# Kernel tuning notes

Measured on AMD Instinct MI355X. Metric: run time of the kernel, lower is better.

## Reference

```python
import jax, jax.numpy as jnp
import numpy as np

NUM_HEADS = 8
DIM_HEAD = 64
SCALE = DIM_HEAD * NUM_HEADS  # q *= dim_head * num_heads, as in the source


def setup_inputs() -> dict:
    key = jax.random.key(0)
    k1, k2, k3, k4 = jax.random.split(key, 4)
    B, C, H, W = 8, 64, 32, 32
    x = jax.random.normal(k1, (B, C, H, W), dtype=jnp.float32)
    # 1x1 conv == matmul over channels; small init keeps post-scale logits sane
    w_qkv = jax.random.normal(k2, (3 * NUM_HEADS * DIM_HEAD, C), dtype=jnp.float32) * 0.02
    rel_h = jax.random.normal(k3, (2 * H - 1, DIM_HEAD), dtype=jnp.float32) * 0.02
    rel_w = jax.random.normal(k4, (2 * W - 1, DIM_HEAD), dtype=jnp.float32) * 0.02
    return {"x": x, "w_qkv": w_qkv, "rel_h": rel_h, "rel_w": rel_w}


def _rel_indices(H, W):
    # flattened 2D grid positions
    pos_y = np.repeat(np.arange(H), W)  # [HW]
    pos_x = np.tile(np.arange(W), H)    # [HW]
    rel_y = pos_y[None, :] - pos_y[:, None] + (H - 1)  # [HW, HW] in [0, 2H-2]
    rel_x = pos_x[None, :] - pos_x[:, None] + (W - 1)  # [HW, HW] in [0, 2W-2]
    return jnp.asarray(rel_y), jnp.asarray(rel_x)


def reference(x, w_qkv, rel_h, rel_w):
    B, C, H, W = x.shape
    n = H * W
    # 1x1 conv (bias=False) -> per-pixel matmul
    xf = x.reshape(B, C, n)                              # b c n
    qkv = jnp.einsum('oc,bcn->bon', w_qkv, xf)           # b (3 h d) n
    q, k, v = jnp.split(qkv, 3, axis=1)
    def to_heads(t):  # b (h d) n -> b h n d
        return t.reshape(B, NUM_HEADS, DIM_HEAD, n).transpose(0, 1, 3, 2)
    q, k, v = to_heads(q), to_heads(k), to_heads(v)
    q = q * SCALE  # scale applied before QK^T AND before pos bias (in-place in torch)

    sim = jnp.einsum('bhid,bhjd->bhij', q, k)            # [B, h, n, n]

    # relative position bias: q_i . rel_h[dy] + q_i . rel_w[dx]
    logits_h = jnp.einsum('bhid,rd->bhir', q, rel_h)     # [B, h, n, 2H-1]
    logits_w = jnp.einsum('bhid,rd->bhir', q, rel_w)     # [B, h, n, 2W-1]
    rel_y, rel_x = _rel_indices(H, W)                    # [n, n] each
    i_idx = jnp.arange(n)[:, None]                       # [n, 1]
    bias = logits_h[:, :, i_idx, rel_y] + logits_w[:, :, i_idx, rel_x]  # [B,h,n,n]

    attn = jax.nn.softmax(sim + bias, axis=-1)
    out = jnp.einsum('bhij,bhjd->bhid', attn, v)         # [B, h, n, d]
    out = out.transpose(0, 1, 3, 2).reshape(B, NUM_HEADS * DIM_HEAD, H, W)
    return out
```

## Files before the change

kernel.cpp:

```cpp
#include <hip/hip_runtime.h>
#include <hip/hip_bf16.h>
#include <hip/hip_fp16.h>

typedef _Float16 h8 __attribute__((ext_vector_type(8)));
typedef _Float16 h2 __attribute__((ext_vector_type(2)));
typedef unsigned short us8 __attribute__((ext_vector_type(8)));
typedef float f4 __attribute__((ext_vector_type(4)));
typedef float f16v __attribute__((ext_vector_type(16)));

#define NH 8
#define DH 64
#define NPIX 1024
#define CIN 64
#define NBH 64
#define QSCALE (512.0f * 1.44269504f)
#define LOSCALE 2048.0f
#define INV_LOSCALE (1.0f / 2048.0f)
#define DTHR 12.0f

__device__ __forceinline__ void gload_lds16(const void* g, void* lds) {
  __builtin_amdgcn_global_load_lds(
      (const __attribute__((address_space(1))) void*)g,
      (__attribute__((address_space(3))) void*)lds, 16, 0, 0);
}

__device__ __forceinline__ float fexp2(float x) {
#if __has_builtin(__builtin_amdgcn_exp2f)
  return __builtin_amdgcn_exp2f(x);
#else
  return exp2f(x);
#endif
}

__device__ __forceinline__ unsigned pk16(float a, float b) {
  auto r = __builtin_amdgcn_cvt_pkrtz(a, b);
  union { decltype(r) h; unsigned u; } x;
  x.h = r;
  return x.u;
}

__global__ __launch_bounds__(256) void qkv_mfma(
    const float* __restrict__ x, const float* __restrict__ wqkv,
    _Float16* __restrict__ Qh, _Float16* __restrict__ Ql,
    _Float16* __restrict__ Kh, _Float16* __restrict__ Kl,
    _Float16* __restrict__ Vv) {
  __shared__ __align__(16) char QS[49152];
  char* Wh = QS;
  char* Wl = QS + 16384;
  char* Xh = QS + 32768;
  char* Xl = QS + 40960;

  const int tid = threadIdx.x;
  const int lane = tid & 63;
  const int w = tid >> 6;
  const int c = lane & 15;
  const int g = lane >> 4;
  const int o0 = blockIdx.x * 128;
  const int p0 = blockIdx.y * 64;
  const int b = blockIdx.z;

  #pragma unroll
  for (int it = 0; it < 4; ++it) {
    int task = tid + it * 256;
    int oct = task & 7, o = task >> 3;
    const f4* wr = (const f4*)(wqkv + (size_t)(o0 + o) * CIN + oct * 8);
    f4 wa = wr[0], wb = wr[1];
    h8 hi, lo;
    #pragma unroll
    for (int e = 0; e < 8; ++e) {
      float v = e < 4 ? wa[e] : wb[e - 4];
      _Float16 h = (_Float16)v;
      hi[e] = h;
      lo[e] = (_Float16)((v - (float)h) * LOSCALE);
    }
    int byo = o * 128 + ((oct ^ (o & 7)) << 4);
    *(h8*)(Wh + byo) = hi;
    *(h8*)(Wl + byo) = lo;
  }
  {
    int kp = tid & 31;
    int pgrp = tid >> 5;
    const float* xr0 = x + ((size_t)b * CIN + 2 * kp) * NPIX + p0 + pgrp * 8;
    const float* xr1 = xr0 + NPIX;
    f4 a0 = *(const f4*)xr0, a1 = *(const f4*)(xr0 + 4);
    f4 b0 = *(const f4*)xr1, b1 = *(const f4*)(xr1 + 4);
    int oct = kp >> 2;
    int slot4 = (kp & 3) * 4;
    #pragma unroll
    for (int e = 0; e < 8; ++e) {
      float v0 = e < 4 ? a0[e] : a1[e - 4];
      float v1 = e < 4 ? b0[e] : b1[e - 4];
      _Float16 h0 = (_Float16)v0, h1 = (_Float16)v1;
      float l0f = (v0 - (float)h0) * LOSCALE;
      float l1f = (v1 - (float)h1) * LOSCALE;
      int p = pgrp * 8 + e;
      int byo = p * 128 + ((oct ^ (p & 7)) << 4) + slot4;
      union { h2 h; unsigned u; } uh, ul;
      uh.h[0] = h0; uh.h[1] = h1;
      ul.h[0] = (_Float16)l0f; ul.h[1] = (_Float16)l1f;
      *(unsigned*)(Xh + byo) = uh.u;
      *(unsigned*)(Xl + byo) = ul.u;
    }
  }
  __syncthreads();

  f4 zf = {0.f, 0.f, 0.f, 0.f};
  f4 acc[2][4], cor[2][4];
  #pragma unroll
  for (int oi = 0; oi < 2; ++oi)
    #pragma unroll
    for (int pi = 0; pi < 4; ++pi) { acc[oi][pi] = zf; cor[oi][pi] = zf; }

  const int ob = w * 32;
  #pragma unroll
  for (int kh = 0; kh < 2; ++kh) {
    h8 ah[2], al[2], bh[4], bl[4];
    #pragma unroll
    for (int oi = 0; oi < 2; ++oi) {
      int orow = ob + ((c >> 2) << 3) + (c & 3) + oi * 4;
      int ch = (((kh * 4 + g) ^ (orow & 7)) << 4);
      ah[oi] = *(const h8*)(Wh + orow * 128 + ch);
      al[oi] = *(const h8*)(Wl + orow * 128 + ch);
    }
    #pragma unroll
    for (int pi = 0; pi < 4; ++pi) {
      int prow = pi * 16 + c;
      int ch = (((kh * 4 + g) ^ (prow & 7)) << 4);
      bh[pi] = *(const h8*)(Xh + prow * 128 + ch);
      bl[pi] = *(const h8*)(Xl + prow * 128 + ch);
    }
    __builtin_amdgcn_s_setprio(1);
    #pragma unroll
    for (int oi = 0; oi < 2; ++oi)
      #pragma unroll
      for (int pi = 0; pi < 4; ++pi) {
        acc[oi][pi] = __builtin_amdgcn_mfma_f32_16x16x32_f16(ah[oi], bh[pi], acc[oi][pi], 0, 0, 0);
        cor[oi][pi] = __builtin_amdgcn_mfma_f32_16x16x32_f16(ah[oi], bl[pi], cor[oi][pi], 0, 0, 0);
        cor[oi][pi] = __builtin_amdgcn_mfma_f32_16x16x32_f16(al[oi], bh[pi], cor[oi][pi], 0, 0, 0);
      }
    __builtin_amdgcn_s_setprio(0);
  }

  const int part = o0 >> 9;
  const float scl = part == 0 ? QSCALE : 1.0f;
  _Float16* dsth = part == 0 ? Qh : (part == 1 ? Kh : Vv);
  _Float16* dstl = part == 0 ? Ql : (part == 1 ? Kl : nullptr);
  #pragma unroll
  for (int pi = 0; pi < 4; ++pi) {
    int obase = o0 + ob + 8 * g;
    int h = (obase >> 6) & 7;
    int d = obase & 63;
    int p_abs = p0 + pi * 16 + c;
    size_t off = (((size_t)(b * NH + h)) * NPIX + p_abs) * DH + d;
    h8 hv, lv;
    #pragma unroll
    for (int oi = 0; oi < 2; ++oi)
      #pragma unroll
      for (int reg = 0; reg < 4; ++reg) {
        float v = (acc[oi][pi][reg] + cor[oi][pi][reg] * INV_LOSCALE) * scl;
        _Float16 hh = (_Float16)v;
        hv[oi * 4 + reg] = hh;
        lv[oi * 4 + reg] = (_Float16)(v - (float)hh);
      }
    *(h8*)(dsth + off) = hv;
    if (dstl) *(h8*)(dstl + off) = lv;
  }
}

__global__ __launch_bounds__(256, 2) void attn_mfma(
    const _Float16* __restrict__ Qh, const _Float16* __restrict__ Ql,
    const _Float16* __restrict__ Kh, const _Float16* __restrict__ Kl,
    const _Float16* __restrict__ V,
    const float* __restrict__ rel_h, const float* __restrict__ rel_w,
    float* __restrict__ out) {
  __shared__ __align__(16) char SMem[73728];
  _Float16* LHc = (_Float16*)(SMem + 65536);
  _Float16* LWT = (_Float16*)(SMem + 32768);
  float* OT = (float*)SMem;

  const int tid = threadIdx.x;
  const int lane = tid & 63;
  const int w = tid >> 6;
  const int wu = __builtin_amdgcn_readfirstlane(w);
  const int c = lane & 15;
  const int g = lane >> 4;
  const int il = lane & 31;
  const int hi = lane >> 5;
  const int bx = blockIdx.x;
  const int bh = ((bx & 7) << 3) | ((bx >> 3) & 7);
  const int i0 = (bx >> 6) << 7;
  char* SPw = SMem + 49152 + w * 4096;

  const _Float16* Qhg = Qh + (size_t)bh * NPIX * DH;
  const _Float16* Qlg = Ql + (size_t)bh * NPIX * DH;
  const _Float16* Khg = Kh + (size_t)bh * NPIX * DH;
  const _Float16* Klg = Kl + (size_t)bh * NPIX * DH;
  const _Float16* Vg  = V  + (size_t)bh * NPIX * DH;

  const h8* Qr0h = (const h8*)(Qhg + (size_t)(i0 + w * 32 + c) * DH);
  const h8* Qr0l = (const h8*)(Qlg + (size_t)(i0 + w * 32 + c) * DH);
  const h8* Qr1h = (const h8*)(Qhg + (size_t)(i0 + w * 32 + 16 + c) * DH);
  const h8* Qr1l = (const h8*)(Qlg + (size_t)(i0 + w * 32 + 16 + c) * DH);
  h8 q0h[2] = {Qr0h[g], Qr0h[4 + g]};
  h8 q0l[2] = {Qr0l[g], Qr0l[4 + g]};
  h8 q1h[2] = {Qr1h[g], Qr1h[4 + g]};
  h8 q1l[2] = {Qr1l[g], Qr1l[4 + g]};

  const int s0i = wu * 128 + lane;
  const int s1i = s0i + 64;
  const int ko0 = (s0i >> 3) * 128 + (((s0i & 7) ^ ((s0i >> 3) & 7)) << 4);
  const int ko1 = (s1i >> 3) * 128 + (((s1i & 7) ^ ((s1i >> 3) & 7)) << 4);

  #pragma unroll
  for (int it = 0; it < 2; ++it) {
    int task = tid + it * 256;
    int oct = task & 7, s = task >> 3;
    int ss = s < 63 ? s : 62;
    const float* sh = rel_h + (size_t)ss * DH + oct * 8;
    const float* sw = rel_w + (size_t)ss * DH + oct * 8;
    h8 hh, ww;
    #pragma unroll
    for (int e = 0; e < 8; ++e) {
      hh[e] = (_Float16)sh[e];
      ww[e] = (_Float16)sw[e];
    }
    int byo = s * 128 + ((oct ^ (s & 7)) << 4);
    *(h8*)(SMem + byo) = hh;
    *(h8*)(SMem + 16384 + byo) = ww;
  }
  __syncthreads();

  const int yi = (i0 + w * 32) >> 5;
  f4 zf = {0.f, 0.f, 0.f, 0.f};
  #pragma unroll
  for (int rs = 0; rs < 2; ++rs) {
    f4 lhD[4], lwD[4];
    #pragma unroll
    for (int st = 0; st < 4; ++st) { lhD[st] = zf; lwD[st] = zf; }
    #pragma unroll
    for (int kh = 0; kh < 2; ++kh) {
      h8 bq = rs ? q1h[kh] : q0h[kh];
      h8 bl = rs ? q1l[kh] : q0l[kh];
      #pragma unroll
      for (int st = 0; st < 4; ++st) {
        int srow = st * 16 + c;
        int chb = srow * 128 + (((kh * 4 + g) ^ (srow & 7)) << 4);
        h8 ra = *(const h8*)(SMem + chb);
        h8 wa = *(const h8*)(SMem + 16384 + chb);
        lhD[st] = __builtin_amdgcn_mfma_f32_16x16x32_f16(ra, bq, lhD[st], 0, 0, 0);
        lhD[st] = __builtin_amdgcn_mfma_f32_16x16x32_f16(ra, bl, lhD[st], 0, 0, 0);
        lwD[st] = __builtin_amdgcn_mfma_f32_16x16x32_f16(wa, bq, lwD[st], 0, 0, 0);
        lwD[st] = __builtin_amdgcn_mfma_f32_16x16x32_f16(wa, bl, lwD[st], 0, 0, 0);
      }
    }
    int lrow = w * 32 + rs * 16 + c;
    #pragma unroll
    for (int st = 0; st < 4; ++st)
      #pragma unroll
      for (int reg = 0; reg < 4; ++reg) {
        int s = st * 16 + 4 * g + reg;
        int k = s - 31 + yi;
        if (k >= 0 && k < 32)
          LHc[(k >> 1) * 256 + lrow * 2 + (k & 1)] = (_Float16)lhD[st][reg];
        LWT[lrow * 64 + s] = (_Float16)lwD[st][reg];
      }
  }
  __syncthreads();

  float lwp[16];
  {
    int r = w * 32 + il;
    #pragma unroll
    for (int reg = 0; reg < 16; ++reg) {
      int jl = (reg & 3) + 8 * (reg >> 2) + 4 * hi;
      lwp[reg] = (float)LWT[r * 64 + 31 + jl - il];
    }
  }
  const h8* Qmh = (const h8*)(Qhg + (size_t)(i0 + w * 32 + il) * DH);
  const h8* Qml = (const h8*)(Qlg + (size_t)(i0 + w * 32 + il) * DH);
  h8 qmh[4], qml[4];
  #pragma unroll
  for (int kb = 0; kb < 4; ++kb) {
    qmh[kb] = Qmh[2 * kb + hi];
    qml[kb] = Qml[2 * kb + hi];
  }
  __syncthreads();

  {
    gload_lds16((const char*)Khg + ko0, SMem + wu * 2048);
    gload_lds16((const char*)Khg + ko1, SMem + wu * 2048 + 1024);
    gload_lds16((const char*)Klg + ko0, SMem + 16384 + wu * 2048);
    gload_lds16((const char*)Klg + ko1, SMem + 16384 + wu * 2048 + 1024);
    int jp = tid & 31, dd = tid >> 5;
    const h8* vr = (const h8*)(Vg + (size_t)(2 * jp) * DH);
    h8 v0 = vr[dd], v1 = vr[8 + dd];
    us8 u0 = *(const us8*)&v0, u1 = *(const us8*)&v1;
    #pragma unroll
    for (int e = 0; e < 8; ++e) {
      int d = dd * 8 + e;
      unsigned int val = (unsigned int)u0[e] | ((unsigned int)u1[e] << 16);
      *(unsigned int*)(SMem + 32768 + d * 128 + (((jp >> 2) ^ (d & 7)) << 4) + (jp & 3) * 4) = val;
    }
  }
  __syncthreads();

  float m_s = -1e30f, lp = 0.f;
  f16v O0 = {0.f}, O1 = {0.f};
  #pragma unroll
  for (int e = 0; e < 16; ++e) { O0[e] = 0.f; O1[e] = 0.f; }

  const int swl = (il & 7);
  int cur = 0;
  #pragma unroll 1
  for (int t = 0; t < 16; ++t) {
    char* Kc  = SMem + cur * 8192;
    char* KLc = SMem + 16384 + cur * 8192;
    char* Vc  = SMem + 32768 + cur * 8192;
    const int nxt = cur ^ 1;
    const bool pre = t < 15;
    const int jp = tid & 31, dd = tid >> 5;
    h8 v0 = {}, v1 = {};
    if (pre) {
      const char* kg  = (const char*)Khg + (size_t)(t + 1) * 8192;
      const char* klg = (const char*)Klg + (size_t)(t + 1) * 8192;
      gload_lds16(kg + ko0, SMem + nxt * 8192 + wu * 2048);
      gload_lds16(kg + ko1, SMem + nxt * 8192 + wu * 2048 + 1024);
      gload_lds16(klg + ko0, SMem + 16384 + nxt * 8192 + wu * 2048);
      gload_lds16(klg + ko1, SMem + 16384 + nxt * 8192 + wu * 2048 + 1024);
      const h8* vr = (const h8*)(Vg + (size_t)((t + 1) * 64 + 2 * jp) * DH);
      v0 = vr[dd];
      v1 = vr[8 + dd];
    }

    f16v S0 = O0 * 0.f, S1 = O0 * 0.f;
    #pragma unroll
    for (int e = 0; e < 16; ++e) { S0[e] = 0.f; S1[e] = 0.f; }
    #pragma unroll
    for (int kb = 0; kb < 4; ++kb) {
      int chb0 = il * 128 + (((2 * kb + hi) ^ swl) << 4);
      int chb1 = chb0 + 32 * 128;
      h8 a0h = *(const h8*)(Kc + chb0);
      h8 a0l = *(const h8*)(KLc + chb0);
      h8 a1h = *(const h8*)(Kc + chb1);
      h8 a1l = *(const h8*)(KLc + chb1);
      __builtin_amdgcn_s_setprio(1);
      S0 = __builtin_amdgcn_mfma_f32_32x32x16_f16(a0h, qmh[kb], S0, 0, 0, 0);
      S0 = __builtin_amdgcn_mfma_f32_32x32x16_f16(a0l, qmh[kb], S0, 0, 0, 0);
      S0 = __builtin_amdgcn_mfma_f32_32x32x16_f16(a0h, qml[kb], S0, 0, 0, 0);
      S1 = __builtin_amdgcn_mfma_f32_32x32x16_f16(a1h, qmh[kb], S1, 0, 0, 0);
      S1 = __builtin_amdgcn_mfma_f32_32x32x16_f16(a1l, qmh[kb], S1, 0, 0, 0);
      S1 = __builtin_amdgcn_mfma_f32_32x32x16_f16(a1h, qml[kb], S1, 0, 0, 0);
      __builtin_amdgcn_s_setprio(0);
    }

    {
      int r = w * 32 + il;
      h2 lhu = *(const h2*)(LHc + t * 256 + r * 2);
      float lh0 = (float)lhu[0], lh1 = (float)lhu[1];
      #pragma unroll
      for (int reg = 0; reg < 16; ++reg) {
        S0[reg] += lwp[reg] + lh0;
        S1[reg] += lwp[reg] + lh1;
      }
      float v8[8];
      #pragma unroll
      for (int e = 0; e < 8; ++e)
        v8[e] = fmaxf(fmaxf(S0[e], S0[e + 8]), fmaxf(S1[e], S1[e + 8]));
      float w0 = fmaxf(fmaxf(v8[0], v8[1]), fmaxf(v8[2], v8[3]));
      float w1 = fmaxf(fmaxf(v8[4], v8[5]), fmaxf(v8[6], v8[7]));
      float mx = fmaxf(w0, w1);
      mx = fmaxf(mx, __shfl_xor(mx, 32, 64));
      bool sk = mx <= m_s + DTHR;
      if (!__all(sk)) {
        float mn = fmaxf(m_s, mx);
        float corr = fexp2(m_s - mn);
        m_s = mn;
        lp *= corr;
        #pragma unroll
        for (int e = 0; e < 16; ++e) { O0[e] *= corr; O1[e] *= corr; }
      }
      float sum = 0.f;
      char* pbse = SPw + il * 128 + hi * 8;
      #pragma unroll
      for (int a = 0; a < 4; ++a) {
        float p0 = fexp2(S0[4 * a + 0] - m_s);
        float p1 = fexp2(S0[4 * a + 1] - m_s);
        float p2 = fexp2(S0[4 * a + 2] - m_s);
        float p3 = fexp2(S0[4 * a + 3] - m_s);
        sum += (p0 + p1) + (p2 + p3);
        *(unsigned long long*)(pbse + ((a ^ swl) << 4)) =
            (unsigned long long)pk16(p0, p1) | ((unsigned long long)pk16(p2, p3) << 32);
      }
      #pragma unroll
      for (int a = 0; a < 4; ++a) {
        float p0 = fexp2(S1[4 * a + 0] - m_s);
        float p1 = fexp2(S1[4 * a + 1] - m_s);
        float p2 = fexp2(S1[4 * a + 2] - m_s);
        float p3 = fexp2(S1[4 * a + 3] - m_s);
        sum += (p0 + p1) + (p2 + p3);
        *(unsigned long long*)(pbse + (((4 + a) ^ swl) << 4)) =
            (unsigned long long)pk16(p0, p1) | ((unsigned long long)pk16(p2, p3) << 32);
      }
      lp += sum;
    }
    __builtin_amdgcn_wave_barrier();

    #pragma unroll
    for (int jkb = 0; jkb < 4; ++jkb) {
      int ci = 2 * jkb + hi;
      int och = ((ci ^ swl) << 4);
      h8 pb = *(const h8*)(SPw + il * 128 + och);
      __builtin_amdgcn_s_setprio(1);
      h8 av0 = *(const h8*)(Vc + il * 128 + och);
      h8 av1 = *(const h8*)(Vc + (32 + il) * 128 + och);
      O0 = __builtin_amdgcn_mfma_f32_32x32x16_f16(av0, pb, O0, 0, 0, 0);
      O1 = __builtin_amdgcn_mfma_f32_32x32x16_f16(av1, pb, O1, 0, 0, 0);
      __builtin_amdgcn_s_setprio(0);
    }

    if (pre) {
      us8 u0 = *(const us8*)&v0, u1 = *(const us8*)&v1;
      char* Vn = SMem + 32768 + nxt * 8192;
      #pragma unroll
      for (int e = 0; e < 8; ++e) {
        int d = dd * 8 + e;
        unsigned int val = (unsigned int)u0[e] | ((unsigned int)u1[e] << 16);
        *(unsigned int*)(Vn + d * 128 + (((jp >> 2) ^ (d & 7)) << 4) + (jp & 3) * 4) = val;
      }
    }
    __syncthreads();
    cur = nxt;
  }

  float lt = lp + __shfl_xor(lp, 32, 64);
  float rr = __builtin_amdgcn_rcpf(lt);
  {
    int r = w * 32 + il;
    #pragma unroll
    for (int reg = 0; reg < 16; ++reg) {
      int dl = (reg & 3) + 8 * (reg >> 2) + 4 * hi;
      int d0 = dl;
      int d1 = 32 + dl;
      OT[d0 * 128 + (r ^ ((d0 & 7) << 3))] = O0[reg] * rr;
      OT[d1 * 128 + (r ^ ((d1 & 7) << 3))] = O1[reg] * rr;
    }
  }
  __syncthreads();
  #pragma unroll
  for (int it = 0; it < 8; ++it) {
    int task = tid + it * 256;
    int rq = task & 31, d = task >> 5;
    f4 vv = *(const f4*)&OT[d * 128 + ((rq * 4) ^ ((d & 7) << 3))];
    *(f4*)(out + (((size_t)bh * 64 + d) << 10) + i0 + rq * 4) = vv;
  }
}

extern "C" void kernel_launch(void* const* d_in, const int* in_sizes, int n_in,
                              void* d_out, int out_size, void* d_ws, size_t ws_size,
                              hipStream_t stream) {
  const float* x  = (const float*)d_in[0];
  const float* wq = (const float*)d_in[1];
  const float* rh = (const float*)d_in[2];
  const float* rw = (const float*)d_in[3];
  float* out = (float*)d_out;

  const size_t sz = (size_t)NBH * NPIX * DH;
  _Float16* Qh = (_Float16*)d_ws;
  _Float16* Ql = Qh + sz;
  _Float16* Kh = Ql + sz;
  _Float16* Kl = Kh + sz;
  _Float16* V  = Kl + sz;

  qkv_mfma<<<dim3(12, 16, 8), 256, 0, stream>>>(x, wq, Qh, Ql, Kh, Kl, V);
  attn_mfma<<<dim3(512), 256, 0, stream>>>(Qh, Ql, Kh, Kl, V, rh, rw, out);
}
```

Before: 76.01 us.

## Build P operand in registers via permlane32 swap; stage QKV stores through LDS

In the attention kernel, the softmax probabilities are now packed to fp16 and redistributed across lane halves with permlane32_swap to form the MFMA B operand directly. This replaces the per-wave LDS round trip (write P, wave barrier, read back) and shrinks shared memory from 72KB to 56KB, which may allow more resident blocks. In the QKV projection kernel, the output tile is transposed through swizzled LDS so each thread writes contiguous 16-byte chunks along d, aiming for better-coalesced global stores at the cost of two extra block barriers.

```diff
diff --git a/kernel.cpp b/kernel.cpp
--- a/kernel.cpp
+++ b/kernel.cpp
@@ -7,6 +7,7 @@
 typedef unsigned short us8 __attribute__((ext_vector_type(8)));
 typedef float f4 __attribute__((ext_vector_type(4)));
 typedef float f16v __attribute__((ext_vector_type(16)));
+typedef int i2v __attribute__((ext_vector_type(2)));
 
 #define NH 8
 #define DH 64
@@ -49,6 +50,8 @@
   char* Wl = QS + 16384;
   char* Xh = QS + 32768;
   char* Xl = QS + 40960;
+  char* Thi = QS;
+  char* Tlo = QS + 16384;
 
   const int tid = threadIdx.x;
   const int lane = tid & 63;
@@ -145,25 +148,45 @@
   const float scl = part == 0 ? QSCALE : 1.0f;
   _Float16* dsth = part == 0 ? Qh : (part == 1 ? Kh : Vv);
   _Float16* dstl = part == 0 ? Ql : (part == 1 ? Kl : nullptr);
-  #pragma unroll
-  for (int pi = 0; pi < 4; ++pi) {
-    int obase = o0 + ob + 8 * g;
-    int h = (obase >> 6) & 7;
-    int d = obase & 63;
-    int p_abs = p0 + pi * 16 + c;
-    size_t off = (((size_t)(b * NH + h)) * NPIX + p_abs) * DH + d;
-    h8 hv, lv;
-    #pragma unroll
-    for (int oi = 0; oi < 2; ++oi)
-      #pragma unroll
-      for (int reg = 0; reg < 4; ++reg) {
-        float v = (acc[oi][pi][reg] + cor[oi][pi][reg] * INV_LOSCALE) * scl;
-        _Float16 hh = (_Float16)v;
-        hv[oi * 4 + reg] = hh;
-        lv[oi * 4 + reg] = (_Float16)(v - (float)hh);
-      }
-    *(h8*)(dsth + off) = hv;
-    if (dstl) *(h8*)(dstl + off) = lv;
+
+  __syncthreads();
+  {
+    const int chunk = 4 * w + g;
+    #pragma unroll
+    for (int pi = 0; pi < 4; ++pi) {
+      int p = pi * 16 + c;
+      h8 hv, lv;
+      #pragma unroll
+      for (int oi = 0; oi < 2; ++oi)
+        #pragma unroll
+        for (int reg = 0; reg < 4; ++reg) {
+          float v = (acc[oi][pi][reg] + cor[oi][pi][reg] * INV_LOSCALE) * scl;
+          _Float16 hh = (_Float16)v;
+          hv[oi * 4 + reg] = hh;
+          lv[oi * 4 + reg] = (_Float16)(v - (float)hh);
+        }
+      int byo = p * 256 + ((chunk ^ (p & 15)) << 4);
+      *(h8*)(Thi + byo) = hv;
+      if (dstl) *(h8*)(Tlo + byo) = lv;
+    }
+  }
+  __syncthreads();
+  #pragma unroll
+  for (int it = 0; it < 4; ++it) {
+    int task = tid + it * 256;
+    int p = task >> 4;
+    int ck = task & 15;
+    int byo = p * 256 + ((ck ^ (p & 15)) << 4);
+    int o = o0 + ck * 8;
+    int h = (o >> 6) & 7;
+    int d = o & 63;
+    size_t off = (((size_t)(b * NH + h)) * NPIX + p0 + p) * DH + d;
+    h8 v = *(const h8*)(Thi + byo);
+    *(h8*)(dsth + off) = v;
+    if (dstl) {
+      h8 v2 = *(const h8*)(Tlo + byo);
+      *(h8*)(dstl + off) = v2;
+    }
   }
 }
 
@@ -173,8 +196,8 @@
     const _Float16* __restrict__ V,
     const float* __restrict__ rel_h, const float* __restrict__ rel_w,
     float* __restrict__ out) {
-  __shared__ __align__(16) char SMem[73728];
-  _Float16* LHc = (_Float16*)(SMem + 65536);
+  __shared__ __align__(16) char SMem[57344];
+  _Float16* LHc = (_Float16*)(SMem + 49152);
   _Float16* LWT = (_Float16*)(SMem + 32768);
   float* OT = (float*)SMem;
 
@@ -189,7 +212,6 @@
   const int bx = blockIdx.x;
   const int bh = ((bx & 7) << 3) | ((bx >> 3) & 7);
   const int i0 = (bx >> 6) << 7;
-  char* SPw = SMem + 49152 + w * 4096;
 
   const _Float16* Qhg = Qh + (size_t)bh * NPIX * DH;
   const _Float16* Qlg = Ql + (size_t)bh * NPIX * DH;
@@ -305,7 +327,7 @@
   __syncthreads();
 
   float m_s = -1e30f, lp = 0.f;
-  f16v O0 = {0.f}, O1 = {0.f};
+  f16v O0, O1;
   #pragma unroll
   for (int e = 0; e < 16; ++e) { O0[e] = 0.f; O1[e] = 0.f; }
 
@@ -332,7 +354,7 @@
       v1 = vr[8 + dd];
     }
 
-    f16v S0 = O0 * 0.f, S1 = O0 * 0.f;
+    f16v S0, S1;
     #pragma unroll
     for (int e = 0; e < 16; ++e) { S0[e] = 0.f; S1[e] = 0.f; }
     #pragma unroll
@@ -353,6 +375,7 @@
       __builtin_amdgcn_s_setprio(0);
     }
 
+    h8 fr[4];
     {
       int r = w * 32 + il;
       h2 lhu = *(const h2*)(LHc + t * 256 + r * 2);
@@ -379,42 +402,42 @@
         #pragma unroll
         for (int e = 0; e < 16; ++e) { O0[e] *= corr; O1[e] *= corr; }
       }
+      float pv0[16], pv1[16];
       float sum = 0.f;
-      char* pbse = SPw + il * 128 + hi * 8;
-      #pragma unroll
-      for (int a = 0; a < 4; ++a) {
-        float p0 = fexp2(S0[4 * a + 0] - m_s);
-        float p1 = fexp2(S0[4 * a + 1] - m_s);
-        float p2 = fexp2(S0[4 * a + 2] - m_s);
-        float p3 = fexp2(S0[4 * a + 3] - m_s);
-        sum += (p0 + p1) + (p2 + p3);
-        *(unsigned long long*)(pbse + ((a ^ swl) << 4)) =
-            (unsigned long long)pk16(p0, p1) | ((unsigned long long)pk16(p2, p3) << 32);
-      }
-      #pragma unroll
-      for (int a = 0; a < 4; ++a) {
-        float p0 = fexp2(S1[4 * a + 0] - m_s);
-        float p1 = fexp2(S1[4 * a + 1] - m_s);
-        float p2 = fexp2(S1[4 * a + 2] - m_s);
-        float p3 = fexp2(S1[4 * a + 3] - m_s);
-        sum += (p0 + p1) + (p2 + p3);
-        *(unsigned long long*)(pbse + (((4 + a) ^ swl) << 4)) =
-            (unsigned long long)pk16(p0, p1) | ((unsigned long long)pk16(p2, p3) << 32);
+      #pragma unroll
+      for (int e = 0; e < 16; ++e) {
+        pv0[e] = fexp2(S0[e] - m_s);
+        pv1[e] = fexp2(S1[e] - m_s);
+        sum += pv0[e] + pv1[e];
       }
       lp += sum;
-    }
-    __builtin_amdgcn_wave_barrier();
+      #pragma unroll
+      for (int jkb = 0; jkb < 4; ++jkb) {
+        const float* pv = (jkb < 2) ? pv0 : pv1;
+        int base = (jkb & 1) * 8;
+        unsigned x01 = pk16(pv[base + 0], pv[base + 1]);
+        unsigned x23 = pk16(pv[base + 2], pv[base + 3]);
+        unsigned y01 = pk16(pv[base + 4], pv[base + 5]);
+        unsigned y23 = pk16(pv[base + 6], pv[base + 7]);
+        i2v r1 = __builtin_amdgcn_permlane32_swap((int)x01, (int)y01, false, false);
+        i2v r2 = __builtin_amdgcn_permlane32_swap((int)x23, (int)y23, false, false);
+        union { unsigned u[4]; h8 h; } fu;
+        fu.u[0] = (unsigned)r1[0];
+        fu.u[1] = (unsigned)r2[0];
+        fu.u[2] = (unsigned)r1[1];
+        fu.u[3] = (unsigned)r2[1];
+        fr[jkb] = fu.h;
+      }
+    }
 
     #pragma unroll
     for (int jkb = 0; jkb < 4; ++jkb) {
-      int ci = 2 * jkb + hi;
-      int och = ((ci ^ swl) << 4);
-      h8 pb = *(const h8*)(SPw + il * 128 + och);
+      int och = (((2 * jkb + hi) ^ swl) << 4);
       __builtin_amdgcn_s_setprio(1);
       h8 av0 = *(const h8*)(Vc + il * 128 + och);
       h8 av1 = *(const h8*)(Vc + (32 + il) * 128 + och);
-      O0 = __builtin_amdgcn_mfma_f32_32x32x16_f16(av0, pb, O0, 0, 0, 0);
-      O1 = __builtin_amdgcn_mfma_f32_32x32x16_f16(av1, pb, O1, 0, 0, 0);
+      O0 = __builtin_amdgcn_mfma_f32_32x32x16_f16(av0, fr[jkb], O0, 0, 0, 0);
+      O1 = __builtin_amdgcn_mfma_f32_32x32x16_f16(av1, fr[jkb], O1, 0, 0, 0);
       __builtin_amdgcn_s_setprio(0);
     }
 
```

New measurement: 72.10 us. -5.1%, faster.
